# Kernel tuning notes

Measured on AMD Instinct MI355X. Metric: run time of the kernel, lower is better.

Reference implementation:

```python
import jax, jax.numpy as jnp
import numpy as np

EPS_RMS = 1e-6
EPS_SCALE = 1e-5


def setup_inputs() -> dict:
    key = jax.random.key(0)
    k1, k2 = jax.random.split(key)
    B, S, D_IN, D_OUT = 4, 2048, 2048, 8192
    x = jax.random.normal(k1, (B, S, D_IN), dtype=jnp.float32)
    # kaiming_uniform-ish init bound
    bound = 1.0 / np.sqrt(D_IN)
    weight = jax.random.uniform(k2, (D_OUT, D_IN), dtype=jnp.float32, minval=-bound, maxval=bound)
    gamma = jnp.ones((D_IN,), dtype=jnp.float32)
    return {"x": x, "weight": weight, "gamma": gamma}


def rmsnorm(x, gamma):
    xf = x.astype(jnp.float32)
    inv = jax.lax.rsqrt(jnp.mean(xf * xf, axis=-1, keepdims=True) + EPS_RMS)
    return (xf * inv).astype(x.dtype) * gamma


def quantize_weights_ternary(weight):
    scale = jnp.maximum(jnp.mean(jnp.abs(weight)), EPS_SCALE)
    wn = weight / scale
    wq = jax.lax.stop_gradient(jnp.round(jnp.clip(wn, -1.0, 1.0)) - wn) + wn  # STE
    return wq, scale


def reference(x, weight, gamma):
    x_norm = rmsnorm(x, gamma)                      # [B, S, D_in]
    wq, scale = quantize_weights_ternary(weight)    # [D_out, D_in], scalar
    out = jnp.einsum('bsd,od->bso', x_norm, wq)     # [B, S, D_out]
    return out * scale
```

## Files before the change

kernel.cpp:

```cpp
#include <hip/hip_runtime.h>
#include <hip/hip_bf16.h>
#include <stdint.h>

#define M_ROWS 8192
#define K_DIM  2048
#define N_DIM  8192
#define W_ELEMS (N_DIM * K_DIM)
#define X_ELEMS (M_ROWS * K_DIM)
#define NT 32

typedef __bf16 v8bf __attribute__((ext_vector_type(8)));
typedef float  v4f  __attribute__((ext_vector_type(4)));

__device__ inline unsigned short f2bf(float f) {
  uint32_t u = __builtin_bit_cast(uint32_t, f);
  uint32_t r = (u + 0x7fffu + ((u >> 16) & 1u)) >> 16;
  return (unsigned short)r;
}

__device__ inline void async_copy16(const void* g, void* l) {
  __builtin_amdgcn_global_load_lds(
      (const __attribute__((address_space(1))) void*)g,
      (__attribute__((address_space(3))) void*)l, 16, 0, 0);
}

__global__ __launch_bounds__(256) void absum_kernel(const float* __restrict__ W,
                                                    double* __restrict__ out) {
  int tid = blockIdx.x * 256 + threadIdx.x;
  int stride = gridDim.x * 256;
  const float4* W4 = (const float4*)W;
  const int n4 = W_ELEMS / 4;
  double acc = 0.0;
  for (int i = tid; i < n4; i += stride) {
    float4 v = W4[i];
    acc += (double)fabsf(v.x) + (double)fabsf(v.y) +
           (double)fabsf(v.z) + (double)fabsf(v.w);
  }
  for (int off = 32; off > 0; off >>= 1) acc += __shfl_down(acc, off);
  __shared__ double wsum[4];
  int lane = threadIdx.x & 63, wid = threadIdx.x >> 6;
  if (lane == 0) wsum[wid] = acc;
  __syncthreads();
  if (threadIdx.x == 0) atomicAdd(out, wsum[0] + wsum[1] + wsum[2] + wsum[3]);
}

__global__ __launch_bounds__(256) void rmsnorm_kernel(const float* __restrict__ X,
                                                      const float* __restrict__ gamma,
                                                      unsigned short* __restrict__ Xn) {
  const int row = blockIdx.x;
  const int t = threadIdx.x;
  const float4* xr = (const float4*)(X + (size_t)row * K_DIM);
  float4 a = xr[t * 2];
  float4 b = xr[t * 2 + 1];
  float ss = a.x * a.x + a.y * a.y + a.z * a.z + a.w * a.w +
             b.x * b.x + b.y * b.y + b.z * b.z + b.w * b.w;
  for (int off = 32; off > 0; off >>= 1) ss += __shfl_down(ss, off);
  __shared__ float wsum[4];
  int lane = t & 63, wid = t >> 6;
  if (lane == 0) wsum[wid] = ss;
  __syncthreads();
  float total = wsum[0] + wsum[1] + wsum[2] + wsum[3];
  float inv = 1.0f / sqrtf(total * (1.0f / (float)K_DIM) + 1e-6f);
  const float4* gr = (const float4*)gamma;
  float4 g0 = gr[t * 2];
  float4 g1 = gr[t * 2 + 1];
  union { unsigned short h[8]; uint4 u; } p;
  p.h[0] = f2bf((a.x * inv) * g0.x);
  p.h[1] = f2bf((a.y * inv) * g0.y);
  p.h[2] = f2bf((a.z * inv) * g0.z);
  p.h[3] = f2bf((a.w * inv) * g0.w);
  p.h[4] = f2bf((b.x * inv) * g1.x);
  p.h[5] = f2bf((b.y * inv) * g1.y);
  p.h[6] = f2bf((b.z * inv) * g1.z);
  p.h[7] = f2bf((b.w * inv) * g1.w);
  ((uint4*)(Xn + (size_t)row * K_DIM))[t] = p.u;
}

__global__ __launch_bounds__(256) void quant_kernel(const float* __restrict__ W,
                                                    const double* __restrict__ sum_ws,
                                                    unsigned short* __restrict__ Wq) {
  float s = (float)fmax(sum_ws[0] * (1.0 / (double)W_ELEMS), 1e-5);
  size_t idx = ((size_t)blockIdx.x * 256 + threadIdx.x) * 8;
  const float4* w4 = (const float4*)(W + idx);
  float4 a = w4[0];
  float4 b = w4[1];
  union { unsigned short h[8]; uint4 u; } p;
  p.h[0] = f2bf(rintf(fminf(1.f, fmaxf(-1.f, a.x / s))));
  p.h[1] = f2bf(rintf(fminf(1.f, fmaxf(-1.f, a.y / s))));
  p.h[2] = f2bf(rintf(fminf(1.f, fmaxf(-1.f, a.z / s))));
  p.h[3] = f2bf(rintf(fminf(1.f, fmaxf(-1.f, a.w / s))));
  p.h[4] = f2bf(rintf(fminf(1.f, fmaxf(-1.f, b.x / s))));
  p.h[5] = f2bf(rintf(fminf(1.f, fmaxf(-1.f, b.y / s))));
  p.h[6] = f2bf(rintf(fminf(1.f, fmaxf(-1.f, b.z / s))));
  p.h[7] = f2bf(rintf(fminf(1.f, fmaxf(-1.f, b.w / s))));
  *(uint4*)(Wq + idx) = p.u;
}

__global__ __launch_bounds__(512, 2) void gemm_kernel(
    const unsigned short* __restrict__ A,
    const unsigned short* __restrict__ B,
    const double* __restrict__ sum_ws,
    float* __restrict__ C) {
  __shared__ __align__(16) char lds[131072];

  const int tid = threadIdx.x;
  const int lane = tid & 63;
  const int wave = tid >> 6;
  const int wm = wave & 1;
  const int wn = wave >> 1;

  const int bid = blockIdx.x;
  const int swz = (bid & 7) * 128 + (bid >> 3);
  const int st = swz >> 4, wi = swz & 15;
  const int mb = (st >> 3) * 4 + (wi >> 2);
  const int nb = (st & 7) * 4 + (wi & 3);
  const int m0 = mb * 256;
  const int n0 = nb * 256;

  const int srow3 = lane >> 3;
  const int scg = (lane & 7) ^ srow3;

  const int aoff_a = wm * 8192 + (lane & 15) * 128;
  const int boff_b = wn * 4096 + (lane & 15) * 128;
  const int swzk0 = ((lane >> 4) ^ (lane & 7)) << 4;
  const int swzk1 = ((4 + (lane >> 4)) ^ (lane & 7)) << 4;

  v4f acc[8][4] = {};
  v8bf af[4][2];
  v8bf b0f[2][2];
  v8bf b1f[2][2];

#define STAGE_A(B_, H_, KT_) do {                                              \
    _Pragma("unroll")                                                          \
    for (int j = 0; j < 2; ++j) {                                              \
      const int chunk_ = wave * 2 + j;                                         \
      const int slot_ = chunk_ * 8 + srow3;                                    \
      const int row_ = ((slot_ >> 6) << 7) + ((H_) << 6) + (slot_ & 63);       \
      async_copy16(A + (size_t)(m0 + row_) * K_DIM + ((KT_) << 6) + (scg << 3),\
                   lds + (B_) * 32768 + (H_) * 16384 + chunk_ * 1024);         \
    } } while (0)

#define STAGE_B(B_, H_, KT_) do {                                              \
    _Pragma("unroll")                                                          \
    for (int j = 0; j < 2; ++j) {                                              \
      const int chunk_ = wave * 2 + j;                                         \
      const int slot_ = chunk_ * 8 + srow3;                                    \
      const int row_ = ((slot_ >> 5) << 6) + ((H_) << 5) + (slot_ & 31);       \
      async_copy16(B + (size_t)(n0 + row_) * K_DIM + ((KT_) << 6) + (scg << 3),\
                   lds + 65536 + (B_) * 32768 + (H_) * 16384 + chunk_ * 1024); \
    } } while (0)

#define LOADA(B_, QM_) do {                                                    \
    _Pragma("unroll")                                                          \
    for (int tm = 0; tm < 4; ++tm) {                                           \
      af[tm][0] = *(const v8bf*)(lds + (B_) * 32768 + (QM_) * 16384 +          \
                                 aoff_a + tm * 2048 + swzk0);                  \
      af[tm][1] = *(const v8bf*)(lds + (B_) * 32768 + (QM_) * 16384 +          \
                                 aoff_a + tm * 2048 + swzk1);                  \
    } } while (0)

#define LOADB(B_, QN_, DST) do {                                               \
    _Pragma("unroll")                                                          \
    for (int tn = 0; tn < 2; ++tn) {                                           \
      DST[tn][0] = *(const v8bf*)(lds + 65536 + (B_) * 32768 + (QN_) * 16384 + \
                                  boff_b + tn * 2048 + swzk0);                 \
      DST[tn][1] = *(const v8bf*)(lds + 65536 + (B_) * 32768 + (QN_) * 16384 + \
                                  boff_b + tn * 2048 + swzk1);                 \
    } } while (0)

#define MMAC(BF, QM_, QN_) do {                                                \
    _Pragma("unroll")                                                          \
    for (int ks = 0; ks < 2; ++ks)                                             \
    _Pragma("unroll")                                                          \
    for (int tm = 0; tm < 4; ++tm)                                             \
    _Pragma("unroll")                                                          \
    for (int tn = 0; tn < 2; ++tn)                                             \
      acc[(QM_) * 4 + tm][(QN_) * 2 + tn] =                                    \
          __builtin_amdgcn_mfma_f32_16x16x32_bf16(                             \
              BF[tn][ks], af[tm][ks],                                          \
              acc[(QM_) * 4 + tm][(QN_) * 2 + tn], 0, 0, 0);                   \
  } while (0)

#define BARRIER() __builtin_amdgcn_s_barrier()
#define VM8() asm volatile("s_waitcnt vmcnt(8)" ::: "memory")

#define TILE(T_, B_) do {                                                      \
    const int t1_ = ((T_) + 1 < NT) ? (T_) + 1 : NT - 1;                       \
    const int t2_ = ((T_) + 2 < NT) ? (T_) + 2 : NT - 1;                       \
                                                            \
    LOADA(B_, 0);                                                              \
    LOADB(B_, 0, b0f);                                                         \
    STAGE_B(1 - (B_), 1, t1_);                                                 \
    BARRIER();                                                                 \
    __builtin_amdgcn_s_setprio(1); MMAC(b0f, 0, 0);                            \
    __builtin_amdgcn_s_setprio(0);                                             \
    VM8(); BARRIER();                                                          \
                                                            \
    LOADB(B_, 1, b1f);                                                         \
    STAGE_A(1 - (B_), 1, t1_);                                                 \
    BARRIER();                                                                 \
    __builtin_amdgcn_s_setprio(1); MMAC(b1f, 0, 1);                            \
    __builtin_amdgcn_s_setprio(0);                                             \
    VM8(); BARRIER();                                                          \
                                                            \
    LOADA(B_, 1);                                                              \
    STAGE_A(B_, 0, t2_);                                                       \
    BARRIER();                                                                 \
    __builtin_amdgcn_s_setprio(1); MMAC(b0f, 1, 0);                            \
    __builtin_amdgcn_s_setprio(0);                                             \
    BARRIER();                                                                 \
                                                            \
    STAGE_B(B_, 0, t2_);                                                       \
    BARRIER();                                                                 \
    __builtin_amdgcn_s_setprio(1); MMAC(b1f, 1, 1);                            \
    __builtin_amdgcn_s_setprio(0);                                             \
    VM8(); BARRIER();                                                          \
  } while (0)

  STAGE_A(0, 0, 0);
  STAGE_B(0, 0, 0);
  STAGE_B(0, 1, 0);
  STAGE_A(0, 1, 0);
  STAGE_A(1, 0, 1);
  STAGE_B(1, 0, 1);
  VM8();
  BARRIER();

  for (int t = 0; t < NT; t += 2) {
    TILE(t, 0);
    TILE(t + 1, 1);
  }

  const float s = (float)fmax(sum_ws[0] * (1.0 / (double)W_ELEMS), 1e-5);
  const int mBase = m0 + wm * 128 + (lane & 15);
  const int nBase = n0 + wn * 64 + ((lane >> 4) << 2);
#pragma unroll
  for (int tm = 0; tm < 8; ++tm) {
#pragma unroll
    for (int tn = 0; tn < 4; ++tn) {
      float4 v;
      v.x = acc[tm][tn][0] * s;
      v.y = acc[tm][tn][1] * s;
      v.z = acc[tm][tn][2] * s;
      v.w = acc[tm][tn][3] * s;
      *(float4*)&C[(size_t)(mBase + tm * 16) * N_DIM + (nBase + tn * 16)] = v;
    }
  }

#undef STAGE_A
#undef STAGE_B
#undef LOADA
#undef LOADB
#undef MMAC
#undef BARRIER
#undef VM8
#undef TILE
}

extern "C" void kernel_launch(void* const* d_in, const int* in_sizes, int n_in,
                              void* d_out, int out_size, void* d_ws, size_t ws_size,
                              hipStream_t stream) {
  const float* x = (const float*)d_in[0];
  const float* w = (const float*)d_in[1];
  const float* gamma = (const float*)d_in[2];
  float* out = (float*)d_out;

  double* ws_sum = (double*)d_ws;
  unsigned short* xn = (unsigned short*)((char*)d_ws + 16);
  unsigned short* wq = (unsigned short*)((char*)d_ws + 16 + (size_t)X_ELEMS * 2);

  hipMemsetAsync(d_ws, 0, 16, stream);
  absum_kernel<<<2048, 256, 0, stream>>>(w, ws_sum);
  rmsnorm_kernel<<<M_ROWS, 256, 0, stream>>>(x, gamma, xn);
  quant_kernel<<<W_ELEMS / (256 * 8), 256, 0, stream>>>(w, ws_sum, wq);
  gemm_kernel<<<(M_ROWS / 256) * (N_DIM / 256), 512, 0, stream>>>(xn, wq, ws_sum, out);
}
```

Baseline: 619.2 us.

## Merge absum and rmsnorm launches, drop atomics, reorder GEMM LDS staging

Merges the weight abs-sum and the RMSNorm row kernels into one launch. The abs-sum blocks now write per-block partials that a tiny reduce kernel folds into a float scale, which removes the memset and the double atomics. Inside the GEMM tile loop the B-fragment loads and A/B stage copies are reordered so that B fragments for the next tile are prefetched early and the waitcnt placement changes. The reordering risks LDS hazards or reduced overlap if the buffer indexing is wrong. Partials reuse the wq buffer before quant overwrites it.

```diff
diff --git a/kernel.cpp b/kernel.cpp
--- a/kernel.cpp
+++ b/kernel.cpp
@@ -8,6 +8,7 @@
 #define W_ELEMS (N_DIM * K_DIM)
 #define X_ELEMS (M_ROWS * K_DIM)
 #define NT 32
+#define ABSUM_BLOCKS 256
 
 typedef __bf16 v8bf __attribute__((ext_vector_type(8)));
 typedef float  v4f  __attribute__((ext_vector_type(4)));
@@ -24,42 +25,44 @@
       (__attribute__((address_space(3))) void*)l, 16, 0, 0);
 }
 
-__global__ __launch_bounds__(256) void absum_kernel(const float* __restrict__ W,
-                                                    double* __restrict__ out) {
-  int tid = blockIdx.x * 256 + threadIdx.x;
-  int stride = gridDim.x * 256;
-  const float4* W4 = (const float4*)W;
-  const int n4 = W_ELEMS / 4;
-  double acc = 0.0;
-  for (int i = tid; i < n4; i += stride) {
-    float4 v = W4[i];
-    acc += (double)fabsf(v.x) + (double)fabsf(v.y) +
-           (double)fabsf(v.z) + (double)fabsf(v.w);
-  }
-  for (int off = 32; off > 0; off >>= 1) acc += __shfl_down(acc, off);
-  __shared__ double wsum[4];
-  int lane = threadIdx.x & 63, wid = threadIdx.x >> 6;
-  if (lane == 0) wsum[wid] = acc;
-  __syncthreads();
-  if (threadIdx.x == 0) atomicAdd(out, wsum[0] + wsum[1] + wsum[2] + wsum[3]);
-}
-
-__global__ __launch_bounds__(256) void rmsnorm_kernel(const float* __restrict__ X,
-                                                      const float* __restrict__ gamma,
-                                                      unsigned short* __restrict__ Xn) {
-  const int row = blockIdx.x;
+__global__ __launch_bounds__(256) void prep_kernel(const float* __restrict__ X,
+                                                   const float* __restrict__ gamma,
+                                                   const float* __restrict__ W,
+                                                   unsigned short* __restrict__ Xn,
+                                                   double* __restrict__ partials) {
+  __shared__ double wsumd[4];
+  __shared__ float wsumf[4];
   const int t = threadIdx.x;
+  const int lane = t & 63, wid = t >> 6;
+
+  if (blockIdx.x < ABSUM_BLOCKS) {
+    const int pb = blockIdx.x;
+    int tid = pb * 256 + t;
+    const float4* W4 = (const float4*)W;
+    const int n4 = W_ELEMS / 4;
+    double acc = 0.0;
+    for (int i = tid; i < n4; i += ABSUM_BLOCKS * 256) {
+      float4 v = W4[i];
+      acc += (double)fabsf(v.x) + (double)fabsf(v.y) +
+             (double)fabsf(v.z) + (double)fabsf(v.w);
+    }
+    for (int off = 32; off > 0; off >>= 1) acc += __shfl_down(acc, off);
+    if (lane == 0) wsumd[wid] = acc;
+    __syncthreads();
+    if (t == 0) partials[pb] = wsumd[0] + wsumd[1] + wsumd[2] + wsumd[3];
+    return;
+  }
+
+  const int row = blockIdx.x - ABSUM_BLOCKS;
   const float4* xr = (const float4*)(X + (size_t)row * K_DIM);
   float4 a = xr[t * 2];
   float4 b = xr[t * 2 + 1];
   float ss = a.x * a.x + a.y * a.y + a.z * a.z + a.w * a.w +
              b.x * b.x + b.y * b.y + b.z * b.z + b.w * b.w;
   for (int off = 32; off > 0; off >>= 1) ss += __shfl_down(ss, off);
-  __shared__ float wsum[4];
-  int lane = t & 63, wid = t >> 6;
-  if (lane == 0) wsum[wid] = ss;
+  if (lane == 0) wsumf[wid] = ss;
   __syncthreads();
-  float total = wsum[0] + wsum[1] + wsum[2] + wsum[3];
+  float total = wsumf[0] + wsumf[1] + wsumf[2] + wsumf[3];
   float inv = 1.0f / sqrtf(total * (1.0f / (float)K_DIM) + 1e-6f);
   const float4* gr = (const float4*)gamma;
   float4 g0 = gr[t * 2];
@@ -76,10 +79,24 @@
   ((uint4*)(Xn + (size_t)row * K_DIM))[t] = p.u;
 }
 
+__global__ __launch_bounds__(256) void reduce_kernel(const double* __restrict__ partials,
+                                                     float* __restrict__ scale) {
+  double v = partials[threadIdx.x];
+  for (int off = 32; off > 0; off >>= 1) v += __shfl_down(v, off);
+  __shared__ double ws[4];
+  int lane = threadIdx.x & 63, wid = threadIdx.x >> 6;
+  if (lane == 0) ws[wid] = v;
+  __syncthreads();
+  if (threadIdx.x == 0) {
+    double total = ws[0] + ws[1] + ws[2] + ws[3];
+    scale[0] = (float)fmax(total * (1.0 / (double)W_ELEMS), 1e-5);
+  }
+}
+
 __global__ __launch_bounds__(256) void quant_kernel(const float* __restrict__ W,
-                                                    const double* __restrict__ sum_ws,
+                                                    const float* __restrict__ scale,
                                                     unsigned short* __restrict__ Wq) {
-  float s = (float)fmax(sum_ws[0] * (1.0 / (double)W_ELEMS), 1e-5);
+  float s = scale[0];
   size_t idx = ((size_t)blockIdx.x * 256 + threadIdx.x) * 8;
   const float4* w4 = (const float4*)(W + idx);
   float4 a = w4[0];
@@ -99,7 +116,7 @@
 __global__ __launch_bounds__(512, 2) void gemm_kernel(
     const unsigned short* __restrict__ A,
     const unsigned short* __restrict__ B,
-    const double* __restrict__ sum_ws,
+    const float* __restrict__ scale,
     float* __restrict__ C) {
   __shared__ __align__(16) char lds[131072];
 
@@ -187,17 +204,15 @@
 #define TILE(T_, B_) do {                                                      \
     const int t1_ = ((T_) + 1 < NT) ? (T_) + 1 : NT - 1;                       \
     const int t2_ = ((T_) + 2 < NT) ? (T_) + 2 : NT - 1;                       \
-                                                            \
+               \
     LOADA(B_, 0);                                                              \
-    LOADB(B_, 0, b0f);                                                         \
-    STAGE_B(1 - (B_), 1, t1_);                                                 \
+    STAGE_A(1 - (B_), 1, t1_);                                                 \
     BARRIER();                                                                 \
     __builtin_amdgcn_s_setprio(1); MMAC(b0f, 0, 0);                            \
     __builtin_amdgcn_s_setprio(0);                                             \
-    VM8(); BARRIER();                                                          \
+    BARRIER();                                                                 \
                                                             \
     LOADB(B_, 1, b1f);                                                         \
-    STAGE_A(1 - (B_), 1, t1_);                                                 \
     BARRIER();                                                                 \
     __builtin_amdgcn_s_setprio(1); MMAC(b1f, 0, 1);                            \
     __builtin_amdgcn_s_setprio(0);                                             \
@@ -205,16 +220,18 @@
                                                             \
     LOADA(B_, 1);                                                              \
     STAGE_A(B_, 0, t2_);                                                       \
+    STAGE_B(B_, 1, t2_);                                                       \
     BARRIER();                                                                 \
     __builtin_amdgcn_s_setprio(1); MMAC(b0f, 1, 0);                            \
     __builtin_amdgcn_s_setprio(0);                                             \
     BARRIER();                                                                 \
-                                                            \
+                  \
     STAGE_B(B_, 0, t2_);                                                       \
-    BARRIER();                                                                 \
+    VM8(); BARRIER();                                                          \
+    LOADB(1 - (B_), 0, b0f);                                                   \
     __builtin_amdgcn_s_setprio(1); MMAC(b1f, 1, 1);                            \
     __builtin_amdgcn_s_setprio(0);                                             \
-    VM8(); BARRIER();                                                          \
+    BARRIER();                                                                 \
   } while (0)
 
   STAGE_A(0, 0, 0);
@@ -222,16 +239,18 @@
   STAGE_B(0, 1, 0);
   STAGE_A(0, 1, 0);
   STAGE_A(1, 0, 1);
+  STAGE_B(1, 1, 1);
   STAGE_B(1, 0, 1);
   VM8();
   BARRIER();
+  LOADB(0, 0, b0f);
 
   for (int t = 0; t < NT; t += 2) {
     TILE(t, 0);
     TILE(t + 1, 1);
   }
 
-  const float s = (float)fmax(sum_ws[0] * (1.0 / (double)W_ELEMS), 1e-5);
+  const float s = scale[0];
   const int mBase = m0 + wm * 128 + (lane & 15);
   const int nBase = n0 + wn * 64 + ((lane >> 4) << 2);
 #pragma unroll
@@ -265,13 +284,13 @@
   const float* gamma = (const float*)d_in[2];
   float* out = (float*)d_out;
 
-  double* ws_sum = (double*)d_ws;
+  float* scale_f = (float*)d_ws;
   unsigned short* xn = (unsigned short*)((char*)d_ws + 16);
   unsigned short* wq = (unsigned short*)((char*)d_ws + 16 + (size_t)X_ELEMS * 2);
-
-  hipMemsetAsync(d_ws, 0, 16, stream);
-  absum_kernel<<<2048, 256, 0, stream>>>(w, ws_sum);
-  rmsnorm_kernel<<<M_ROWS, 256, 0, stream>>>(x, gamma, xn);
-  quant_kernel<<<W_ELEMS / (256 * 8), 256, 0, stream>>>(w, ws_sum, wq);
-  gemm_kernel<<<(M_ROWS / 256) * (N_DIM / 256), 512, 0, stream>>>(xn, wq, ws_sum, out);
-}
+  double* partials = (double*)wq;
+
+  prep_kernel<<<ABSUM_BLOCKS + M_ROWS, 256, 0, stream>>>(x, gamma, w, xn, partials);
+  reduce_kernel<<<1, 256, 0, stream>>>(partials, scale_f);
+  quant_kernel<<<W_ELEMS / (256 * 8), 256, 0, stream>>>(w, scale_f, wq);
+  gemm_kernel<<<(M_ROWS / 256) * (N_DIM / 256), 512, 0, stream>>>(xn, wq, scale_f, out);
+}
```

New measurement: 611.5 us. No clear change (-1.2%).
